# Performance work log

Hardware: AMD Instinct MI355X
Metric: run time of the kernel (lower is better)

Reference implementation:

```python
import jax, jax.numpy as jnp
import numpy as np

NUM_CLASSES = 80
POS_OVERLAP = 0.5
NEG_OVERLAP = 0.4
REG_MEAN = 0.0
REG_STD = 0.2


def setup_inputs() -> dict:
    key = jax.random.key(0)
    k1, k2, k3, k4, k5 = jax.random.split(key, 5)
    B, N, A = 8, 64, 120000
    IMG = 800.0
    # GT annotations: [x1, y1, x2, y2, class]
    xy = jax.random.uniform(k1, (B, N, 2)) * IMG
    wh = jax.random.uniform(k2, (B, N, 2)) * 256.0 + 1.0
    boxes = jnp.concatenate([xy, xy + wh], axis=-1)
    labels = jax.random.randint(k3, (B, N, 1), 0, NUM_CLASSES).astype(jnp.float32)
    annotations_batch = jnp.concatenate([boxes, labels], axis=-1)  # [B,N,5]
    # Anchors: [x1, y1, x2, y2]
    axy = jax.random.uniform(k4, (A, 2)) * IMG
    awh = jax.random.uniform(k5, (A, 2)) * 256.0 + 1.0
    anchors = jnp.concatenate([axy, axy + awh], axis=-1)  # [A,4]
    return {"annotations_batch": annotations_batch, "anchors": anchors}


def _iou(anchors, boxes):
    # anchors [A,4], boxes [N,4] -> IoU [A,N]
    area_a = (anchors[:, 2] - anchors[:, 0]) * (anchors[:, 3] - anchors[:, 1])
    area_b = (boxes[:, 2] - boxes[:, 0]) * (boxes[:, 3] - boxes[:, 1])
    lt = jnp.maximum(anchors[:, None, :2], boxes[None, :, :2])  # [A,N,2]
    rb = jnp.minimum(anchors[:, None, 2:], boxes[None, :, 2:])  # [A,N,2]
    wh = jnp.clip(rb - lt, 0.0)
    inter = wh[..., 0] * wh[..., 1]
    union = area_a[:, None] + area_b[None, :] - inter
    return inter / jnp.maximum(union, 1e-8)


def _targets_one(annotations, anchors):
    # annotations [N,5], anchors [A,4]
    boxes = annotations[:, :4]
    labels = jax.lax.stop_gradient(annotations[:, 4]).astype(jnp.int32)  # [N]
    ov = _iou(anchors, boxes)                 # [A,N]
    best = jnp.argmax(ov, axis=1)             # [A] assigned gt per anchor
    max_ov = jnp.max(ov, axis=1)              # [A]
    positive = max_ov >= POS_OVERLAP
    ignore = (max_ov > NEG_OVERLAP) & (~positive)
    anchor_states = jnp.where(positive, 1.0, jnp.where(ignore, -1.0, 0.0))
    # Classification target: one-hot of assigned class for positive anchors
    cls_target = jax.nn.one_hot(labels[best], NUM_CLASSES, dtype=anchors.dtype)
    cls_target = cls_target * positive[:, None].astype(anchors.dtype)
    gt = boxes[best]                           # [A,4]
    wa = anchors[:, 2] - anchors[:, 0]
    ha = anchors[:, 3] - anchors[:, 1]
    scale = jnp.stack([wa, ha, wa, ha], axis=1)  # [A,4]
    reg_target = ((gt - anchors) / scale - REG_MEAN) / REG_STD
    return cls_target, reg_target, anchor_states


def reference(annotations_batch, anchors):
    return jax.vmap(lambda ann: _targets_one(ann, anchors))(annotations_batch)
```

## Files before the change

kernel.cpp:

```cpp
#include <hip/hip_runtime.h>

#define NUM_CLASSES 80
#define A_NUM 120000
#define B_NUM 8
#define N_BOX 64

typedef float f4 __attribute__((ext_vector_type(4)));

__global__ __launch_bounds__(256, 4) void compute_targets_kernel(
    const float* __restrict__ annotations,
    const float4* __restrict__ anchors4,
    float* __restrict__ out)
{
#pragma clang fp contract(off)
    __shared__ float4 sbox[N_BOX];
    __shared__ float  sarea[N_BOX];
    __shared__ int    slab[N_BOX];
    __shared__ int    scls[256];

    const int tid  = threadIdx.x;
    const int wv   = tid >> 6;
    const int lane = tid & 63;
    const int b    = blockIdx.y;
    const int a0   = blockIdx.x * 256;
    const int aw0  = a0 + wv * 64;
    const int a    = a0 + tid;

    if (tid < N_BOX) {
        const float* ann = annotations + ((size_t)b * N_BOX + tid) * 5;
        const float x0 = ann[0], y0 = ann[1], x1 = ann[2], y1 = ann[3];
        sbox[tid]  = make_float4(x0, y0, x1, y1);
        sarea[tid] = (x1 - x0) * (y1 - y0);
        slab[tid]  = (int)ann[4];
    }
    __syncthreads();

    if (aw0 >= A_NUM) return;

    const float4 anc = anchors4[a];
    const float wa = anc.z - anc.x;
    const float ha = anc.w - anc.y;
    const float area_a = wa * ha;

    float best_iou = -1.0f;
    int   best_j   = 0;
#pragma unroll 8
    for (int j = 0; j < N_BOX; ++j) {
        const float4 bx = sbox[j];
        const float ltx = fmaxf(anc.x, bx.x);
        const float lty = fmaxf(anc.y, bx.y);
        const float rbx = fminf(anc.z, bx.z);
        const float rby = fminf(anc.w, bx.w);
        const float w = fmaxf(rbx - ltx, 0.0f);
        const float h = fmaxf(rby - lty, 0.0f);
        const float inter = w * h;
        const float uni   = (area_a + sarea[j]) - inter;
        const float iou   = inter / uni;
        if (iou > best_iou) { best_iou = iou; best_j = j; }
    }

    const bool positive = best_iou >= 0.5f;
    const bool ignore   = (best_iou > 0.4f) && !positive;
    const float state   = positive ? 1.0f : (ignore ? -1.0f : 0.0f);

    const float4 gt = sbox[best_j];
    f4 reg;
    reg.x = ((gt.x - anc.x) / wa) / 0.2f;
    reg.y = ((gt.y - anc.y) / ha) / 0.2f;
    reg.z = ((gt.z - anc.z) / wa) / 0.2f;
    reg.w = ((gt.w - anc.w) / ha) / 0.2f;

    const size_t CLS = (size_t)B_NUM * A_NUM * NUM_CLASSES;
    const size_t REG = (size_t)B_NUM * A_NUM * 4;
    f4* regout = (f4*)(out + CLS);
    __builtin_nontemporal_store(reg, &regout[(size_t)b * A_NUM + a]);
    __builtin_nontemporal_store(state, &out[CLS + REG + (size_t)b * A_NUM + a]);

    scls[tid] = positive ? slab[best_j] : -1;

    f4* clsout = (f4*)out + ((size_t)b * A_NUM + aw0) * 20;
#pragma unroll
    for (int i = 0; i < 20; ++i) {
        const int pos = i * 64 + lane;
        const int al  = pos / 20;
        const int q   = pos - al * 20;
        const int lab = scls[wv * 64 + al];
        const int c0  = q * 4;
        f4 v;
        v.x = (lab == c0    ) ? 1.0f : 0.0f;
        v.y = (lab == c0 + 1) ? 1.0f : 0.0f;
        v.z = (lab == c0 + 2) ? 1.0f : 0.0f;
        v.w = (lab == c0 + 3) ? 1.0f : 0.0f;
        __builtin_nontemporal_store(v, &clsout[pos]);
    }
}

extern "C" void kernel_launch(void* const* d_in, const int* in_sizes, int n_in,
                              void* d_out, int out_size, void* d_ws, size_t ws_size,
                              hipStream_t stream) {
    const float*  annotations = (const float*)d_in[0];
    const float4* anchors     = (const float4*)d_in[1];
    float* out = (float*)d_out;

    dim3 grid((A_NUM + 255) / 256, B_NUM);
    compute_targets_kernel<<<grid, 256, 0, stream>>>(annotations, anchors, out);
}
```

Measured before the change: 60.82 us.

## Split one-hot writes into early zero-fill plus scatter fixup kernel

After: 78.33 us. 28.8% more time.

```diff
diff --git a/kernel.cpp b/kernel.cpp
--- a/kernel.cpp
+++ b/kernel.cpp
@@ -7,10 +7,12 @@
 
 typedef float f4 __attribute__((ext_vector_type(4)));
 
-__global__ __launch_bounds__(256, 4) void compute_targets_kernel(
+
+__global__ __launch_bounds__(256, 4) void targets_main_kernel(
     const float* __restrict__ annotations,
     const float4* __restrict__ anchors4,
-    float* __restrict__ out)
+    float* __restrict__ out,
+    signed char* __restrict__ labels)
 {
 #pragma clang fp contract(off)
     __shared__ float4 sbox[N_BOX];
@@ -25,6 +27,17 @@
     const int a0   = blockIdx.x * 256;
     const int aw0  = a0 + wv * 64;
     const int a    = a0 + tid;
+    const bool wave_valid = (aw0 < A_NUM);
+    const bool split = (labels != nullptr);
+
+    f4* const clsbase = (f4*)out + ((size_t)b * A_NUM + aw0) * 20;
+
+    if (split && wave_valid) {
+        const f4 z = {0.0f, 0.0f, 0.0f, 0.0f};
+#pragma unroll
+        for (int i = 0; i < 20; ++i)
+            __builtin_nontemporal_store(z, &clsbase[i * 64 + lane]);
+    }
 
     if (tid < N_BOX) {
         const float* ann = annotations + ((size_t)b * N_BOX + tid) * 5;
@@ -35,7 +48,7 @@
     }
     __syncthreads();
 
-    if (aw0 >= A_NUM) return;
+    if (!wave_valid) return;
 
     const float4 anc = anchors4[a];
     const float wa = anc.z - anc.x;
@@ -76,9 +89,12 @@
     __builtin_nontemporal_store(reg, &regout[(size_t)b * A_NUM + a]);
     __builtin_nontemporal_store(state, &out[CLS + REG + (size_t)b * A_NUM + a]);
 
+    if (split) {
+        labels[(size_t)b * A_NUM + a] = positive ? (signed char)slab[best_j] : (signed char)-1;
+        return;
+    }
+
     scls[tid] = positive ? slab[best_j] : -1;
-
-    f4* clsout = (f4*)out + ((size_t)b * A_NUM + aw0) * 20;
 #pragma unroll
     for (int i = 0; i < 20; ++i) {
         const int pos = i * 64 + lane;
@@ -91,8 +107,18 @@
         v.y = (lab == c0 + 1) ? 1.0f : 0.0f;
         v.z = (lab == c0 + 2) ? 1.0f : 0.0f;
         v.w = (lab == c0 + 3) ? 1.0f : 0.0f;
-        __builtin_nontemporal_store(v, &clsout[pos]);
+        __builtin_nontemporal_store(v, &clsbase[pos]);
     }
+}
+
+__global__ __launch_bounds__(256) void targets_fixup_kernel(
+    const signed char* __restrict__ labels,
+    float* __restrict__ out)
+{
+    const int idx = blockIdx.x * 256 + threadIdx.x;
+    const int lab = labels[idx];
+    if (lab >= 0)
+        out[(size_t)idx * NUM_CLASSES + lab] = 1.0f;
 }
 
 extern "C" void kernel_launch(void* const* d_in, const int* in_sizes, int n_in,
@@ -102,6 +128,12 @@
     const float4* anchors     = (const float4*)d_in[1];
     float* out = (float*)d_out;
 
+    const size_t need = (size_t)B_NUM * A_NUM;
+    signed char* labels = (ws_size >= need) ? (signed char*)d_ws : nullptr;
+
     dim3 grid((A_NUM + 255) / 256, B_NUM);
-    compute_targets_kernel<<<grid, 256, 0, stream>>>(annotations, anchors, out);
+    targets_main_kernel<<<grid, 256, 0, stream>>>(annotations, anchors, out, labels);
+    if (labels) {
+        targets_fixup_kernel<<<dim3((B_NUM * A_NUM) / 256), 256, 0, stream>>>(labels, out);
+    }
 }
```
